# Optimization experiments

Measured on AMD Instinct MI355X. Metric: run time of the kernel, lower is better.

Reference implementation:

```python
import jax, jax.numpy as jnp
import numpy as np

N = 100000      # num_nodes
E = 1600000     # num_edges
D_IN = 256      # input_dim
H = 64          # hidden_dim
OUT = 32        # output_dim
EMB = 128       # node2vec embedding_dim
HEADS = 2       # GAT heads (concat=False -> mean over heads)
NEG_SLOPE = 0.2 # GATConv leaky_relu default


def setup_inputs() -> dict:
    key = jax.random.key(0)
    ks = jax.random.split(key, 24)
    s = lambda k, shape, fan: (jax.random.normal(k, shape, jnp.float32) * (1.0 / np.sqrt(fan)))
    return {
        "x": jax.random.normal(ks[0], (N, D_IN), jnp.float32),
        "edge_index": jax.random.randint(ks[1], (2, E), 0, N, jnp.int64),
        # frozen node2vec embedding table (used under no_grad in the original)
        "n2v_emb": jax.random.normal(ks[2], (N, EMB), jnp.float32),
        "n2v_proj_w": s(ks[3], (EMB, H), EMB), "n2v_proj_b": jnp.zeros((H,), jnp.float32),
        "input_proj_w": s(ks[4], (D_IN + H, H), D_IN + H), "input_proj_b": jnp.zeros((H,), jnp.float32),
        "gate_w": s(ks[5], (D_IN + H, H), D_IN + H), "gate_b": jnp.zeros((H,), jnp.float32),
        # SAGEConv layers: out = mean_agg(x_j) @ wl + bl + x @ wr
        "sage0_wl": s(ks[6], (H, H), H), "sage0_bl": jnp.zeros((H,), jnp.float32), "sage0_wr": s(ks[7], (H, H), H),
        "sage1_wl": s(ks[8], (H, H), H), "sage1_bl": jnp.zeros((H,), jnp.float32), "sage1_wr": s(ks[9], (H, H), H),
        # GATConv(H, H, heads=2, concat=False)
        "gat_w": s(ks[10], (H, HEADS * H), H),
        "gat_att_src": s(ks[11], (HEADS, H), H), "gat_att_dst": s(ks[12], (HEADS, H), H),
        "gat_b": jnp.zeros((H,), jnp.float32),
        "fin_wl": s(ks[13], (H, OUT), H), "fin_bl": jnp.zeros((OUT,), jnp.float32), "fin_wr": s(ks[14], (H, OUT), H),
    }


def _sage(h, src, dst, wl, bl, wr, n):
    # PyG SAGEConv with mean aggregation: lin_l(mean_j h_j) + lin_r(h_i)
    msum = jax.ops.segment_sum(h[src], dst, num_segments=n)
    deg = jax.ops.segment_sum(jnp.ones((src.shape[0],), h.dtype), dst, num_segments=n)
    agg = msum / jnp.maximum(deg, 1.0)[:, None]
    return agg @ wl + bl + h @ wr


def _gat(h, src, dst, w, att_src, att_dst, b, n):
    # GATConv with self-loops (PyG default), heads averaged (concat=False)
    loops = jnp.arange(n, dtype=src.dtype)
    src = jnp.concatenate([src, loops]); dst = jnp.concatenate([dst, loops])
    xh = (h @ w).reshape(n, HEADS, H)                     # [n, heads, H]
    a_src = jnp.einsum('nhd,hd->nh', xh, att_src)         # [n, heads]
    a_dst = jnp.einsum('nhd,hd->nh', xh, att_dst)
    e = jax.nn.leaky_relu(a_src[src] + a_dst[dst], NEG_SLOPE)  # [E', heads]
    emax = jax.ops.segment_max(e, dst, num_segments=n)
    ex = jnp.exp(e - emax[dst])
    esum = jax.ops.segment_sum(ex, dst, num_segments=n)
    alpha = ex / (esum[dst] + 1e-16)                      # edge softmax per dst, per head
    out = jax.ops.segment_sum(alpha[:, :, None] * xh[src], dst, num_segments=n)
    return out.mean(axis=1) + b                           # [n, H]


def reference(x, edge_index, n2v_emb, n2v_proj_w, n2v_proj_b, input_proj_w, input_proj_b,
              gate_w, gate_b, sage0_wl, sage0_bl, sage0_wr, sage1_wl, sage1_bl, sage1_wr,
              gat_w, gat_att_src, gat_att_dst, gat_b, fin_wl, fin_bl, fin_wr):
    n = x.shape[0]
    src, dst = edge_index[0], edge_index[1]
    # node2vec embeddings are frozen (torch.no_grad in original)
    n2v = jax.lax.stop_gradient(n2v_emb)
    n2v_p = n2v @ n2v_proj_w + n2v_proj_b                 # [n, H]
    combined = jnp.concatenate([x, n2v_p], axis=-1)       # [n, D_IN+H]
    gate = jax.nn.sigmoid(combined @ gate_w + gate_b)
    x_proj = combined @ input_proj_w + input_proj_b
    raw_proj = jnp.concatenate([x, jnp.zeros((n, H), x.dtype)], axis=-1) @ input_proj_w + input_proj_b
    h = gate * x_proj + (1.0 - gate) * raw_proj           # node_indices=None -> all nodes
    h = jax.nn.relu(_sage(h, src, dst, sage0_wl, sage0_bl, sage0_wr, n))
    h = jax.nn.relu(_sage(h, src, dst, sage1_wl, sage1_bl, sage1_wr, n))
    h = jax.nn.relu(_gat(h, src, dst, gat_w, gat_att_src, gat_att_dst, gat_b, n))
    return _sage(h, src, dst, fin_wl, fin_bl, fin_wr, n)  # [n, OUT]
```

## Files before the change

### kernel.cpp

```cpp
#include <hip/hip_runtime.h>
#include <math.h>

#define NN 100000
#define NE 1600000
#define DIN 256
#define HD 64
#define OUTD 32
#define EMBD 128
#define SLOPE 0.2f
#define AST 68
#define NT ((NN + 63) / 64)
#define SCHUNK 1024
#define SNBLK ((NN + SCHUNK - 1) / SCHUNK)

__device__ __forceinline__ float lrelu(float x) { return x > 0.f ? x : SLOPE * x; }
__device__ __forceinline__ ushort f2b(float f) {
    unsigned u = __float_as_uint(f);
    return (ushort)((u + 0x7FFFu + ((u >> 16) & 1u)) >> 16);
}
__device__ __forceinline__ float b2f(ushort v) { return __uint_as_float(((unsigned)v) << 16); }

__global__ void k_count(const int* __restrict__ dst, int* __restrict__ cnt) {
    int i = blockIdx.x * blockDim.x + threadIdx.x;
    if (i < NE) atomicAdd(&cnt[dst[i]], 1);
}

__global__ __launch_bounds__(256) void k_scan1(const int* __restrict__ cnt,
                                               int* __restrict__ rowptr,
                                               int* __restrict__ blksum) {
    __shared__ int ts[256];
    int base = blockIdx.x * SCHUNK + threadIdx.x * 4;
    int v0 = 0, v1 = 0, v2 = 0, v3 = 0;
    if (base < NN)     v0 = cnt[base];
    if (base + 1 < NN) v1 = cnt[base + 1];
    if (base + 2 < NN) v2 = cnt[base + 2];
    if (base + 3 < NN) v3 = cnt[base + 3];
    int s = v0 + v1 + v2 + v3;
    ts[threadIdx.x] = s;
    __syncthreads();
    for (int off = 1; off < 256; off <<= 1) {
        int w = (threadIdx.x >= off) ? ts[threadIdx.x - off] : 0;
        __syncthreads();
        ts[threadIdx.x] += w;
        __syncthreads();
    }
    int excl = ts[threadIdx.x] - s;
    if (base < NN)     rowptr[base]     = excl;
    if (base + 1 < NN) rowptr[base + 1] = excl + v0;
    if (base + 2 < NN) rowptr[base + 2] = excl + v0 + v1;
    if (base + 3 < NN) rowptr[base + 3] = excl + v0 + v1 + v2;
    if (threadIdx.x == 255) blksum[blockIdx.x] = ts[255];
}

__global__ __launch_bounds__(128) void k_scan2(int* __restrict__ blksum) {
    __shared__ int ts[128];
    int t = threadIdx.x;
    int v = (t < SNBLK) ? blksum[t] : 0;
    ts[t] = v;
    __syncthreads();
    for (int off = 1; off < 128; off <<= 1) {
        int w = (t >= off) ? ts[t - off] : 0;
        __syncthreads();
        ts[t] += w;
        __syncthreads();
    }
    if (t < SNBLK) blksum[t] = ts[t] - v;
}

__global__ void k_scan3(const int* __restrict__ blksum, const int* __restrict__ cnt,
                        int* __restrict__ rowptr, int* __restrict__ cursor,
                        float* __restrict__ invdeg) {
    int i = blockIdx.x * blockDim.x + threadIdx.x;
    if (i < NN) {
        int v = rowptr[i] + blksum[i >> 10];
        rowptr[i] = v;
        cursor[i] = v;
        invdeg[i] = 1.0f / fmaxf((float)cnt[i], 1.0f);
    }
    if (i == 0) rowptr[NN] = NE;
}

__global__ void k_fill(const int* __restrict__ src, const int* __restrict__ dst,
                       int* __restrict__ cursor, int* __restrict__ colsrc) {
    int i = blockIdx.x * blockDim.x + threadIdx.x;
    if (i >= NE) return;
    int pos = atomicAdd(&cursor[dst[i]], 1);
    colsrc[pos] = src[i];
}

__device__ __forceinline__ void stageA(const float* __restrict__ g, int nbase, int ldg, int koff,
                                       float (*As)[AST]) {
    for (int i = threadIdx.x; i < 1024; i += 256) {
        int m = i >> 4, k4 = (i & 15) << 2;
        int row = nbase + m;
        if (row >= NN) row = NN - 1;
        *(float4*)&As[m][k4] = *(const float4*)&g[(size_t)row * ldg + koff + k4];
    }
}
__device__ __forceinline__ void stageW(const float* __restrict__ g, float* Ws) {
    for (int i = threadIdx.x; i < 1024; i += 256) ((float4*)Ws)[i] = ((const float4*)g)[i];
}
__device__ __forceinline__ void stageWcols(const float* __restrict__ g, int ldg, int coff,
                                           float* Ws) {
    for (int i = threadIdx.x; i < 1024; i += 256) {
        int r = i >> 4, c4 = (i & 15) << 2;
        *(float4*)&Ws[r * 64 + c4] = *(const float4*)&g[r * ldg + coff + c4];
    }
}
__device__ __forceinline__ void mac16v(const float (*As)[AST], const float* __restrict__ Ws,
                                       float (*acc)[4], int tr, int tc) {
#pragma unroll 4
    for (int k4 = 0; k4 < 64; k4 += 4) {
        float4 a0 = *(const float4*)&As[tr * 4 + 0][k4];
        float4 a1 = *(const float4*)&As[tr * 4 + 1][k4];
        float4 a2 = *(const float4*)&As[tr * 4 + 2][k4];
        float4 a3 = *(const float4*)&As[tr * 4 + 3][k4];
#pragma unroll
        for (int j = 0; j < 4; j++) {
            float4 w = *(const float4*)&Ws[(k4 + j) * 64 + tc * 4];
            float e0 = (&a0.x)[j], e1 = (&a1.x)[j], e2 = (&a2.x)[j], e3 = (&a3.x)[j];
            acc[0][0] += e0 * w.x; acc[0][1] += e0 * w.y; acc[0][2] += e0 * w.z; acc[0][3] += e0 * w.w;
            acc[1][0] += e1 * w.x; acc[1][1] += e1 * w.y; acc[1][2] += e1 * w.z; acc[1][3] += e1 * w.w;
            acc[2][0] += e2 * w.x; acc[2][1] += e2 * w.y; acc[2][2] += e2 * w.z; acc[2][3] += e2 * w.w;
            acc[3][0] += e3 * w.x; acc[3][1] += e3 * w.y; acc[3][2] += e3 * w.z; acc[3][3] += e3 * w.w;
        }
    }
}

__global__ __launch_bounds__(256) void k_n2vp_t(const float* __restrict__ n2v,
                                                const float* __restrict__ w,
                                                const float* __restrict__ b,
                                                float* __restrict__ n2vp) {
    __shared__ float As[64][AST];
    __shared__ float Ws[64 * 64];
    int nbase = blockIdx.x * 64;
    int tc = threadIdx.x & 15, tr = threadIdx.x >> 4;
    float acc[4][4] = {};
    for (int c = 0; c < 2; c++) {
        if (c) __syncthreads();
        stageA(n2v, nbase, EMBD, c * 64, As);
        stageW(w + c * 64 * 64, Ws);
        __syncthreads();
        mac16v(As, Ws, acc, tr, tc);
    }
    float b0 = b[tc * 4], b1 = b[tc * 4 + 1], b2 = b[tc * 4 + 2], b3 = b[tc * 4 + 3];
#pragma unroll
    for (int i = 0; i < 4; i++) {
        int row = nbase + tr * 4 + i;
        if (row < NN) {
            float4 o = {acc[i][0] + b0, acc[i][1] + b1, acc[i][2] + b2, acc[i][3] + b3};
            *(float4*)&n2vp[(size_t)row * HD + tc * 4] = o;
        }
    }
}

__global__ __launch_bounds__(256) void k_front_t(const float* __restrict__ x,
                                                 const float* __restrict__ n2vp,
                                                 const float* __restrict__ ip_w,
                                                 const float* __restrict__ ip_b,
                                                 const float* __restrict__ gate_w,
                                                 const float* __restrict__ gate_b,
                                                 float* __restrict__ h0,
                                                 ushort* __restrict__ h0b) {
    __shared__ float As[64][AST];
    __shared__ float Ws[64 * 64];
    int nbase = blockIdx.x * 64;
    int tc = threadIdx.x & 15, tr = threadIdx.x >> 4;
    float araw[4][4] = {}, ag[4][4] = {}, adel[4][4] = {};
    for (int c = 0; c < 4; c++) {
        if (c) __syncthreads();
        stageA(x, nbase, DIN, c * 64, As);
        stageW(ip_w + c * 64 * 64, Ws);
        __syncthreads();
        mac16v(As, Ws, araw, tr, tc);
        __syncthreads();
        stageW(gate_w + c * 64 * 64, Ws);
        __syncthreads();
        mac16v(As, Ws, ag, tr, tc);
    }
    __syncthreads();
    stageA(n2vp, nbase, HD, 0, As);
    stageW(ip_w + DIN * 64, Ws);
    __syncthreads();
    mac16v(As, Ws, adel, tr, tc);
    __syncthreads();
    stageW(gate_w + DIN * 64, Ws);
    __syncthreads();
    mac16v(As, Ws, ag, tr, tc);

    float ib0 = ip_b[tc * 4], ib1 = ip_b[tc * 4 + 1], ib2 = ip_b[tc * 4 + 2], ib3 = ip_b[tc * 4 + 3];
    float gb0 = gate_b[tc * 4], gb1 = gate_b[tc * 4 + 1], gb2 = gate_b[tc * 4 + 2], gb3 = gate_b[tc * 4 + 3];
#pragma unroll
    for (int i = 0; i < 4; i++) {
        int row = nbase + tr * 4 + i;
        if (row < NN) {
            float r0 = araw[i][0] + ib0, r1 = araw[i][1] + ib1, r2 = araw[i][2] + ib2, r3 = araw[i][3] + ib3;
            float s0 = 1.f / (1.f + __expf(-(ag[i][0] + gb0)));
            float s1 = 1.f / (1.f + __expf(-(ag[i][1] + gb1)));
            float s2 = 1.f / (1.f + __expf(-(ag[i][2] + gb2)));
            float s3 = 1.f / (1.f + __expf(-(ag[i][3] + gb3)));
            float4 o = {r0 + s0 * adel[i][0], r1 + s1 * adel[i][1],
                        r2 + s2 * adel[i][2], r3 + s3 * adel[i][3]};
            *(float4*)&h0[(size_t)row * HD + tc * 4] = o;
            ushort4 ob = {f2b(o.x), f2b(o.y), f2b(o.z), f2b(o.w)};
            *(ushort4*)&h0b[(size_t)row * HD + tc * 4] = ob;
        }
    }
}

__global__ void k_gather_mean(const int* __restrict__ rowptr, const int* __restrict__ colsrc,
                              const float* __restrict__ invdeg, const ushort* __restrict__ hb,
                              float* __restrict__ agg) {
    int t = threadIdx.x & 63;
    int lane = t & 31, half = t >> 5;
    int gw = blockIdx.x * (blockDim.x >> 6) + (threadIdx.x >> 6);
    int stride = gridDim.x * (blockDim.x >> 6);
    for (int n = gw; n < NN; n += stride) {
        int bg = rowptr[n], en = rowptr[n + 1];
        float a0 = 0.f, a1 = 0.f;
        int i = bg + half;
        for (; i + 6 < en; i += 8) {
            int sa = colsrc[i], sb = colsrc[i + 2], sc = colsrc[i + 4], sd = colsrc[i + 6];
            ushort2 va = *(const ushort2*)&hb[(size_t)sa * HD + lane * 2];
            ushort2 vb = *(const ushort2*)&hb[(size_t)sb * HD + lane * 2];
            ushort2 vc = *(const ushort2*)&hb[(size_t)sc * HD + lane * 2];
            ushort2 vd = *(const ushort2*)&hb[(size_t)sd * HD + lane * 2];
            a0 += b2f(va.x) + b2f(vb.x) + b2f(vc.x) + b2f(vd.x);
            a1 += b2f(va.y) + b2f(vb.y) + b2f(vc.y) + b2f(vd.y);
        }
        for (; i < en; i += 2) {
            int s = colsrc[i];
            ushort2 v = *(const ushort2*)&hb[(size_t)s * HD + lane * 2];
            a0 += b2f(v.x);
            a1 += b2f(v.y);
        }
        a0 += __shfl_xor(a0, 32);
        a1 += __shfl_xor(a1, 32);
        if (half == 0) {
            float id = invdeg[n];
            float2 o = {a0 * id, a1 * id};
            *(float2*)&agg[(size_t)n * HD + lane * 2] = o;
        }
    }
}

__global__ __launch_bounds__(256) void k_sage_t(const float* __restrict__ agg,
                                                const float* __restrict__ h,
                                                const float* __restrict__ wl,
                                                const float* __restrict__ bl,
                                                const float* __restrict__ wr,
                                                float* __restrict__ hout,
                                                ushort* __restrict__ houtb) {
    __shared__ float As[64][AST];
    __shared__ float Ws[64 * 64];
    int nbase = blockIdx.x * 64;
    int tc = threadIdx.x & 15, tr = threadIdx.x >> 4;
    float acc[4][4] = {};
    stageA(agg, nbase, HD, 0, As);
    stageW(wl, Ws);
    __syncthreads();
    mac16v(As, Ws, acc, tr, tc);
    __syncthreads();
    stageA(h, nbase, HD, 0, As);
    stageW(wr, Ws);
    __syncthreads();
    mac16v(As, Ws, acc, tr, tc);
    float b0 = bl[tc * 4], b1 = bl[tc * 4 + 1], b2 = bl[tc * 4 + 2], b3 = bl[tc * 4 + 3];
#pragma unroll
    for (int i = 0; i < 4; i++) {
        int row = nbase + tr * 4 + i;
        if (row < NN) {
            float4 o = {fmaxf(acc[i][0] + b0, 0.f), fmaxf(acc[i][1] + b1, 0.f),
                        fmaxf(acc[i][2] + b2, 0.f), fmaxf(acc[i][3] + b3, 0.f)};
            *(float4*)&hout[(size_t)row * HD + tc * 4] = o;
            ushort4 ob = {f2b(o.x), f2b(o.y), f2b(o.z), f2b(o.w)};
            *(ushort4*)&houtb[(size_t)row * HD + tc * 4] = ob;
        }
    }
}

__global__ __launch_bounds__(256) void k_gatxh_t(const float* __restrict__ h,
                                                 const float* __restrict__ w,
                                                 const float* __restrict__ att_s,
                                                 const float* __restrict__ att_d,
                                                 ushort* __restrict__ xhb,
                                                 float* __restrict__ a_s,
                                                 float* __restrict__ a_d) {
    __shared__ float As[64][AST];
    __shared__ float Ws[64 * 64];
    int nbase = blockIdx.x * 64;
    int tc = threadIdx.x & 15, tr = threadIdx.x >> 4;
    stageA(h, nbase, HD, 0, As);
#pragma unroll
    for (int half = 0; half < 2; half++) {
        if (half) __syncthreads();
        stageWcols(w, 128, half * 64, Ws);
        __syncthreads();
        float acc[4][4] = {};
        mac16v(As, Ws, acc, tr, tc);
        float as0 = att_s[half * 64 + tc * 4], as1 = att_s[half * 64 + tc * 4 + 1];
        float as2 = att_s[half * 64 + tc * 4 + 2], as3 = att_s[half * 64 + tc * 4 + 3];
        float ad0 = att_d[half * 64 + tc * 4], ad1 = att_d[half * 64 + tc * 4 + 1];
        float ad2 = att_d[half * 64 + tc * 4 + 2], ad3 = att_d[half * 64 + tc * 4 + 3];
#pragma unroll
        for (int i = 0; i < 4; i++) {
            int row = nbase + tr * 4 + i;
            float ps = acc[i][0] * as0 + acc[i][1] * as1 + acc[i][2] * as2 + acc[i][3] * as3;
            float pd = acc[i][0] * ad0 + acc[i][1] * ad1 + acc[i][2] * ad2 + acc[i][3] * ad3;
#pragma unroll
            for (int off = 8; off; off >>= 1) {
                ps += __shfl_xor(ps, off);
                pd += __shfl_xor(pd, off);
            }
            if (row < NN) {
                ushort4 ob = {f2b(acc[i][0]), f2b(acc[i][1]), f2b(acc[i][2]), f2b(acc[i][3])};
                *(ushort4*)&xhb[(size_t)row * 128 + half * 64 + tc * 4] = ob;
                if (tc == 0) {
                    a_s[row * 2 + half] = ps;
                    a_d[row * 2 + half] = pd;
                }
            }
        }
    }
}

__global__ void k_gat_fused(const int* __restrict__ rowptr, const int* __restrict__ colsrc,
                            const float* __restrict__ a_s, const float* __restrict__ a_d,
                            const ushort* __restrict__ xhb, const float* __restrict__ gb,
                            float* __restrict__ hout) {
    int t = threadIdx.x & 63;
    int lane = t & 31, half = t >> 5;
    int bl4 = (lane & 15) * 4;
    float4 bias4 = *(const float4*)&gb[bl4];
    int gw = blockIdx.x * (blockDim.x >> 6) + (threadIdx.x >> 6);
    int stride = gridDim.x * (blockDim.x >> 6);
    for (int n = gw; n < NN; n += stride) {
        int bg = rowptr[n], en = rowptr[n + 1];
        float ad0 = a_d[n * 2], ad1 = a_d[n * 2 + 1];
        float a0 = 0.f, a1 = 0.f, a2 = 0.f, a3 = 0.f;
        float ss0 = 0.f, ss1 = 0.f;
        int i = bg + half;
        for (; i + 2 < en; i += 4) {
            int sa = colsrc[i], sb = colsrc[i + 2];
            float2 ava = *(const float2*)&a_s[sa * 2];
            float2 avb = *(const float2*)&a_s[sb * 2];
            ushort4 xva = *(const ushort4*)&xhb[(size_t)sa * 128 + lane * 4];
            ushort4 xvb = *(const ushort4*)&xhb[(size_t)sb * 128 + lane * 4];
            float wa0 = __expf(lrelu(ava.x + ad0));
            float wa1 = __expf(lrelu(ava.y + ad1));
            float wb0 = __expf(lrelu(avb.x + ad0));
            float wb1 = __expf(lrelu(avb.y + ad1));
            ss0 += wa0 + wb0;
            ss1 += wa1 + wb1;
            float wsa = (lane < 16) ? wa0 : wa1;
            float wsb = (lane < 16) ? wb0 : wb1;
            a0 += wsa * b2f(xva.x) + wsb * b2f(xvb.x);
            a1 += wsa * b2f(xva.y) + wsb * b2f(xvb.y);
            a2 += wsa * b2f(xva.z) + wsb * b2f(xvb.z);
            a3 += wsa * b2f(xva.w) + wsb * b2f(xvb.w);
        }
        for (; i < en; i += 2) {
            int s = colsrc[i];
            float2 av = *(const float2*)&a_s[s * 2];
            float w0 = __expf(lrelu(av.x + ad0));
            float w1 = __expf(lrelu(av.y + ad1));
            ss0 += w0;
            ss1 += w1;
            float wsel = (lane < 16) ? w0 : w1;
            ushort4 xv = *(const ushort4*)&xhb[(size_t)s * 128 + lane * 4];
            a0 += wsel * b2f(xv.x);
            a1 += wsel * b2f(xv.y);
            a2 += wsel * b2f(xv.z);
            a3 += wsel * b2f(xv.w);
        }
        if (half == 0) {
            float2 av = *(const float2*)&a_s[n * 2];
            float w0 = __expf(lrelu(av.x + ad0));
            float w1 = __expf(lrelu(av.y + ad1));
            ss0 += w0;
            ss1 += w1;
            float wsel = (lane < 16) ? w0 : w1;
            ushort4 xv = *(const ushort4*)&xhb[(size_t)n * 128 + lane * 4];
            a0 += wsel * b2f(xv.x);
            a1 += wsel * b2f(xv.y);
            a2 += wsel * b2f(xv.z);
            a3 += wsel * b2f(xv.w);
        }
        ss0 += __shfl_xor(ss0, 32);
        ss1 += __shfl_xor(ss1, 32);
        a0 += __shfl_xor(a0, 32);
        a1 += __shfl_xor(a1, 32);
        a2 += __shfl_xor(a2, 32);
        a3 += __shfl_xor(a3, 32);
        float r = (lane < 16) ? (0.5f / (ss0 + 1e-16f)) : (0.5f / (ss1 + 1e-16f));
        float v0 = a0 * r, v1 = a1 * r, v2 = a2 * r, v3 = a3 * r;
        float p0 = __shfl_xor(v0, 16);
        float p1 = __shfl_xor(v1, 16);
        float p2 = __shfl_xor(v2, 16);
        float p3 = __shfl_xor(v3, 16);
        if (half == 0 && lane < 16) {
            float4 o = {fmaxf(v0 + p0 + bias4.x, 0.f), fmaxf(v1 + p1 + bias4.y, 0.f),
                        fmaxf(v2 + p2 + bias4.z, 0.f), fmaxf(v3 + p3 + bias4.w, 0.f)};
            *(float4*)&hout[(size_t)n * HD + lane * 4] = o;
        }
    }
}

__global__ void k_pfin(const float* __restrict__ h, const float* __restrict__ wl,
                       ushort* __restrict__ Pb) {
    __shared__ float sw[HD * OUTD];
    for (int i = threadIdx.x; i < HD * OUTD; i += blockDim.x) sw[i] = wl[i];
    __syncthreads();
    int t = threadIdx.x & 63;
    int c = t & 31, half = t >> 5;
    int gw = blockIdx.x * (blockDim.x >> 6) + (threadIdx.x >> 6);
    int stride = gridDim.x * (blockDim.x >> 6);
    for (int n = gw; n < NN; n += stride) {
        float hv = h[(size_t)n * HD + t];
        float acc = 0.f;
#pragma unroll 8
        for (int i = 0; i < 32; i++) {
            float bb = __shfl(hv, half * 32 + i);
            acc += bb * sw[half * 1024 + i * 32 + c];
        }
        acc += __shfl_xor(acc, 32);
        if (half == 0) Pb[(size_t)n * OUTD + c] = f2b(acc);
    }
}

__global__ void k_final_fused(const int* __restrict__ rowptr, const int* __restrict__ colsrc,
                              const float* __restrict__ invdeg, const ushort* __restrict__ Pb,
                              const float* __restrict__ h, const float* __restrict__ bl,
                              const float* __restrict__ wr, float* __restrict__ out) {
    __shared__ float sw[HD * OUTD];
    for (int i = threadIdx.x; i < HD * OUTD; i += blockDim.x) sw[i] = wr[i];
    __syncthreads();
    int t = threadIdx.x & 63;
    int j = t & 31, half = t >> 5;
    int quarter = t >> 4, lane16 = t & 15;
    float bias = bl[j];
    int gw = blockIdx.x * (blockDim.x >> 6) + (threadIdx.x >> 6);
    int stride = gridDim.x * (blockDim.x >> 6);
    for (int n = gw; n < NN; n += stride) {
        int bg = rowptr[n], en = rowptr[n + 1];
        float a0 = 0.f, a1 = 0.f;
        int i = bg + quarter;
        for (; i + 4 < en; i += 8) {
            int sa = colsrc[i], sb = colsrc[i + 4];
            ushort2 va = *(const ushort2*)&Pb[(size_t)sa * OUTD + lane16 * 2];
            ushort2 vb = *(const ushort2*)&Pb[(size_t)sb * OUTD + lane16 * 2];
            a0 += b2f(va.x) + b2f(vb.x);
            a1 += b2f(va.y) + b2f(vb.y);
        }
        for (; i < en; i += 4) {
            int s = colsrc[i];
            ushort2 v = *(const ushort2*)&Pb[(size_t)s * OUTD + lane16 * 2];
            a0 += b2f(v.x);
            a1 += b2f(v.y);
        }
        a0 += __shfl_xor(a0, 32);
        a1 += __shfl_xor(a1, 32);
        a0 += __shfl_xor(a0, 16);
        a1 += __shfl_xor(a1, 16);
        float hv = h[(size_t)n * HD + t];
        float o = 0.f;
#pragma unroll 8
        for (int i2 = 0; i2 < 32; i2++) {
            float bb = __shfl(hv, half * 32 + i2);
            o += bb * sw[half * 1024 + i2 * 32 + j];
        }
        o += __shfl_xor(o, 32);
        float ga = __shfl(a0, j >> 1);
        float gb_ = __shfl(a1, j >> 1);
        float gv = (j & 1) ? gb_ : ga;
        if (half == 0) out[(size_t)n * OUTD + j] = gv * invdeg[n] + bias + o;
    }
}

extern "C" void kernel_launch(void* const* d_in, const int* in_sizes, int n_in,
                              void* d_out, int out_size, void* d_ws, size_t ws_size,
                              hipStream_t stream) {
    const float* x      = (const float*)d_in[0];
    const int*   eidx   = (const int*)d_in[1];
    const float* n2v    = (const float*)d_in[2];
    const float* n2v_w  = (const float*)d_in[3];
    const float* n2v_b  = (const float*)d_in[4];
    const float* ip_w   = (const float*)d_in[5];
    const float* ip_b   = (const float*)d_in[6];
    const float* gate_w = (const float*)d_in[7];
    const float* gate_b = (const float*)d_in[8];
    const float* s0_wl  = (const float*)d_in[9];
    const float* s0_bl  = (const float*)d_in[10];
    const float* s0_wr  = (const float*)d_in[11];
    const float* s1_wl  = (const float*)d_in[12];
    const float* s1_bl  = (const float*)d_in[13];
    const float* s1_wr  = (const float*)d_in[14];
    const float* gat_w  = (const float*)d_in[15];
    const float* att_s  = (const float*)d_in[16];
    const float* att_d  = (const float*)d_in[17];
    const float* gat_b  = (const float*)d_in[18];
    const float* f_wl   = (const float*)d_in[19];
    const float* f_bl   = (const float*)d_in[20];
    const float* f_wr   = (const float*)d_in[21];

    const int* src = eidx;
    const int* dst = eidx + NE;

    float*  ws     = (float*)d_ws;
    float*  invdeg = ws;
    float*  S1     = invdeg + NN;
    float*  S2     = S1 + (size_t)NN * HD;
    float*  SA     = S2 + (size_t)NN * HD;
    float*  a_s    = SA + (size_t)NN * HD;
    float*  a_d    = a_s + (size_t)NN * 2;
    ushort* Pb     = (ushort*)(a_d + (size_t)NN * 2);
    ushort* hb     = Pb + (size_t)NN * OUTD;
    ushort* xhb    = hb + (size_t)NN * HD;
    int*    cnt    = (int*)(xhb + (size_t)NN * 128);
    int*    rowptr = cnt + NN;
    int*    cursor = rowptr + NN + 1;
    int*    blksum = cursor + NN;
    int*    colsrc = blksum + 128;

    float* n2vp = SA;
    float* agg  = SA;
    float* out  = (float*)d_out;

    const int BT = 256;
    dim3 b128(128), b256(BT);
    int eblk = (NE + BT - 1) / BT;
    int nblk = (NN + BT - 1) / BT;

    hipMemsetAsync(cnt, 0, (size_t)NN * 4, stream);
    k_count<<<eblk, b256, 0, stream>>>(dst, cnt);
    k_scan1<<<SNBLK, b256, 0, stream>>>(cnt, rowptr, blksum);
    k_scan2<<<1, b128, 0, stream>>>(blksum);
    k_scan3<<<nblk, b256, 0, stream>>>(blksum, cnt, rowptr, cursor, invdeg);
    k_fill<<<eblk, b256, 0, stream>>>(src, dst, cursor, colsrc);

    k_n2vp_t<<<NT, b256, 0, stream>>>(n2v, n2v_w, n2v_b, n2vp);
    k_front_t<<<NT, b256, 0, stream>>>(x, n2vp, ip_w, ip_b, gate_w, gate_b, S2, hb);

    k_gather_mean<<<2048, b256, 0, stream>>>(rowptr, colsrc, invdeg, hb, agg);
    k_sage_t<<<NT, b256, 0, stream>>>(agg, S2, s0_wl, s0_bl, s0_wr, S1, hb);

    k_gather_mean<<<2048, b256, 0, stream>>>(rowptr, colsrc, invdeg, hb, agg);
    k_sage_t<<<NT, b256, 0, stream>>>(agg, S1, s1_wl, s1_bl, s1_wr, S2, hb);

    k_gatxh_t<<<NT, b256, 0, stream>>>(S2, gat_w, att_s, att_d, xhb, a_s, a_d);
    k_gat_fused<<<2048, b256, 0, stream>>>(rowptr, colsrc, a_s, a_d, xhb, gat_b, S1);

    k_pfin<<<2048, b256, 0, stream>>>(S1, f_wl, Pb);
    k_final_fused<<<2048, b256, 0, stream>>>(rowptr, colsrc, invdeg, Pb, S1, f_bl, f_wr, out);
}
```

Measured before the change: 758.0 us.

## Use split-bf16 MFMA for the front input-projection and gate GEMMs

Rewrites the front projection kernel to use 16x16x32 bf16 MFMA instructions in place of scalar FP32 multiply-accumulate. Each operand is split into a high and a low bf16 part, and three MFMAs per product (hi*hi, hi*lo, lo*hi) keep accuracy close to FP32. The goal is to take this roughly 100000x320x128 GEMM off the vector ALUs. In exchange, every block converts the weights to bf16 again, and the epilogue writes scalar values in a column-strided pattern rather than float4 rows, which may cost some store efficiency.

After: 709.3 us. 6.4% less time.

```diff
diff --git a/kernel.cpp b/kernel.cpp
--- a/kernel.cpp
+++ b/kernel.cpp
@@ -12,6 +12,10 @@
 #define NT ((NN + 63) / 64)
 #define SCHUNK 1024
 #define SNBLK ((NN + SCHUNK - 1) / SCHUNK)
+
+typedef __attribute__((ext_vector_type(8))) short bf16x8;
+typedef __attribute__((ext_vector_type(8))) unsigned short u16x8;
+typedef __attribute__((ext_vector_type(4))) float f32x4;
 
 __device__ __forceinline__ float lrelu(float x) { return x > 0.f ? x : SLOPE * x; }
 __device__ __forceinline__ ushort f2b(float f) {
@@ -162,48 +166,146 @@
                                                  const float* __restrict__ gate_b,
                                                  float* __restrict__ h0,
                                                  ushort* __restrict__ h0b) {
-    __shared__ float As[64][AST];
-    __shared__ float Ws[64 * 64];
+    __shared__ ushort Ah[64][40], Al[64][40];
+    __shared__ ushort Bih[64][40], Bil[64][40];
+    __shared__ ushort Bgh[64][40], Bgl[64][40];
     int nbase = blockIdx.x * 64;
-    int tc = threadIdx.x & 15, tr = threadIdx.x >> 4;
-    float araw[4][4] = {}, ag[4][4] = {}, adel[4][4] = {};
-    for (int c = 0; c < 4; c++) {
+    int tid = threadIdx.x;
+    int w = tid >> 6, l = tid & 63;
+    int lr = l & 15, lg = l >> 4, lk = lg * 8;
+    f32x4 zero = {0.f, 0.f, 0.f, 0.f};
+    f32x4 araw[4], ag[4], adel[4];
+#pragma unroll
+    for (int t = 0; t < 4; t++) { araw[t] = zero; ag[t] = zero; adel[t] = zero; }
+
+    int arow = tid >> 2, ak0 = (tid & 3) << 3;
+    int garow = nbase + arow;
+    if (garow >= NN) garow = NN - 1;
+
+    for (int c = 0; c < 8; c++) {
         if (c) __syncthreads();
-        stageA(x, nbase, DIN, c * 64, As);
-        stageW(ip_w + c * 64 * 64, Ws);
-        __syncthreads();
-        mac16v(As, Ws, araw, tr, tc);
-        __syncthreads();
-        stageW(gate_w + c * 64 * 64, Ws);
-        __syncthreads();
-        mac16v(As, Ws, ag, tr, tc);
-    }
-    __syncthreads();
-    stageA(n2vp, nbase, HD, 0, As);
-    stageW(ip_w + DIN * 64, Ws);
-    __syncthreads();
-    mac16v(As, Ws, adel, tr, tc);
-    __syncthreads();
-    stageW(gate_w + DIN * 64, Ws);
-    __syncthreads();
-    mac16v(As, Ws, ag, tr, tc);
-
-    float ib0 = ip_b[tc * 4], ib1 = ip_b[tc * 4 + 1], ib2 = ip_b[tc * 4 + 2], ib3 = ip_b[tc * 4 + 3];
-    float gb0 = gate_b[tc * 4], gb1 = gate_b[tc * 4 + 1], gb2 = gate_b[tc * 4 + 2], gb3 = gate_b[tc * 4 + 3];
-#pragma unroll
-    for (int i = 0; i < 4; i++) {
-        int row = nbase + tr * 4 + i;
-        if (row < NN) {
-            float r0 = araw[i][0] + ib0, r1 = araw[i][1] + ib1, r2 = araw[i][2] + ib2, r3 = araw[i][3] + ib3;
-            float s0 = 1.f / (1.f + __expf(-(ag[i][0] + gb0)));
-            float s1 = 1.f / (1.f + __expf(-(ag[i][1] + gb1)));
-            float s2 = 1.f / (1.f + __expf(-(ag[i][2] + gb2)));
-            float s3 = 1.f / (1.f + __expf(-(ag[i][3] + gb3)));
-            float4 o = {r0 + s0 * adel[i][0], r1 + s1 * adel[i][1],
-                        r2 + s2 * adel[i][2], r3 + s3 * adel[i][3]};
-            *(float4*)&h0[(size_t)row * HD + tc * 4] = o;
-            ushort4 ob = {f2b(o.x), f2b(o.y), f2b(o.z), f2b(o.w)};
-            *(ushort4*)&h0b[(size_t)row * HD + tc * 4] = ob;
+        {
+            const float* src = &x[(size_t)garow * DIN + c * 32 + ak0];
+            u16x8 th, tl;
+#pragma unroll
+            for (int u = 0; u < 8; u++) {
+                float v = src[u];
+                ushort h = f2b(v);
+                th[u] = h;
+                tl[u] = f2b(v - b2f(h));
+            }
+            *(u16x8*)&Ah[arow][ak0] = th;
+            *(u16x8*)&Al[arow][ak0] = tl;
+        }
+        {
+            const float* pi = &ip_w[(size_t)(c * 32 + w * 8) * 64 + l];
+            const float* pg = &gate_w[(size_t)(c * 32 + w * 8) * 64 + l];
+            u16x8 ih, il, gh, gl2;
+#pragma unroll
+            for (int u = 0; u < 8; u++) {
+                float v = pi[u * 64];
+                ushort h = f2b(v);
+                ih[u] = h; il[u] = f2b(v - b2f(h));
+                float g = pg[u * 64];
+                ushort hg = f2b(g);
+                gh[u] = hg; gl2[u] = f2b(g - b2f(hg));
+            }
+            *(u16x8*)&Bih[l][w * 8] = ih;
+            *(u16x8*)&Bil[l][w * 8] = il;
+            *(u16x8*)&Bgh[l][w * 8] = gh;
+            *(u16x8*)&Bgl[l][w * 8] = gl2;
+        }
+        __syncthreads();
+        bf16x8 ah = *(const bf16x8*)&Ah[w * 16 + lr][lk];
+        bf16x8 al = *(const bf16x8*)&Al[w * 16 + lr][lk];
+#pragma unroll
+        for (int t = 0; t < 4; t++) {
+            int col = t * 16 + lr;
+            bf16x8 bih = *(const bf16x8*)&Bih[col][lk];
+            bf16x8 bil = *(const bf16x8*)&Bil[col][lk];
+            bf16x8 bgh = *(const bf16x8*)&Bgh[col][lk];
+            bf16x8 bgl = *(const bf16x8*)&Bgl[col][lk];
+            f32x4 r = araw[t];
+            r = __builtin_amdgcn_mfma_f32_16x16x32_bf16(ah, bih, r, 0, 0, 0);
+            r = __builtin_amdgcn_mfma_f32_16x16x32_bf16(ah, bil, r, 0, 0, 0);
+            r = __builtin_amdgcn_mfma_f32_16x16x32_bf16(al, bih, r, 0, 0, 0);
+            araw[t] = r;
+            f32x4 g = ag[t];
+            g = __builtin_amdgcn_mfma_f32_16x16x32_bf16(ah, bgh, g, 0, 0, 0);
+            g = __builtin_amdgcn_mfma_f32_16x16x32_bf16(ah, bgl, g, 0, 0, 0);
+            g = __builtin_amdgcn_mfma_f32_16x16x32_bf16(al, bgh, g, 0, 0, 0);
+            ag[t] = g;
+        }
+    }
+    for (int c = 0; c < 2; c++) {
+        __syncthreads();
+        {
+            const float* src = &n2vp[(size_t)garow * HD + c * 32 + ak0];
+            u16x8 th, tl;
+#pragma unroll
+            for (int u = 0; u < 8; u++) {
+                float v = src[u];
+                ushort h = f2b(v);
+                th[u] = h;
+                tl[u] = f2b(v - b2f(h));
+            }
+            *(u16x8*)&Ah[arow][ak0] = th;
+            *(u16x8*)&Al[arow][ak0] = tl;
+        }
+        {
+            const float* pi = &ip_w[(size_t)(DIN + c * 32 + w * 8) * 64 + l];
+            const float* pg = &gate_w[(size_t)(DIN + c * 32 + w * 8) * 64 + l];
+            u16x8 ih, il, gh, gl2;
+#pragma unroll
+            for (int u = 0; u < 8; u++) {
+                float v = pi[u * 64];
+                ushort h = f2b(v);
+                ih[u] = h; il[u] = f2b(v - b2f(h));
+                float g = pg[u * 64];
+                ushort hg = f2b(g);
+                gh[u] = hg; gl2[u] = f2b(g - b2f(hg));
+            }
+            *(u16x8*)&Bih[l][w * 8] = ih;
+            *(u16x8*)&Bil[l][w * 8] = il;
+            *(u16x8*)&Bgh[l][w * 8] = gh;
+            *(u16x8*)&Bgl[l][w * 8] = gl2;
+        }
+        __syncthreads();
+        bf16x8 ah = *(const bf16x8*)&Ah[w * 16 + lr][lk];
+        bf16x8 al = *(const bf16x8*)&Al[w * 16 + lr][lk];
+#pragma unroll
+        for (int t = 0; t < 4; t++) {
+            int col = t * 16 + lr;
+            bf16x8 bih = *(const bf16x8*)&Bih[col][lk];
+            bf16x8 bil = *(const bf16x8*)&Bil[col][lk];
+            bf16x8 bgh = *(const bf16x8*)&Bgh[col][lk];
+            bf16x8 bgl = *(const bf16x8*)&Bgl[col][lk];
+            f32x4 r = adel[t];
+            r = __builtin_amdgcn_mfma_f32_16x16x32_bf16(ah, bih, r, 0, 0, 0);
+            r = __builtin_amdgcn_mfma_f32_16x16x32_bf16(ah, bil, r, 0, 0, 0);
+            r = __builtin_amdgcn_mfma_f32_16x16x32_bf16(al, bih, r, 0, 0, 0);
+            adel[t] = r;
+            f32x4 g = ag[t];
+            g = __builtin_amdgcn_mfma_f32_16x16x32_bf16(ah, bgh, g, 0, 0, 0);
+            g = __builtin_amdgcn_mfma_f32_16x16x32_bf16(ah, bgl, g, 0, 0, 0);
+            g = __builtin_amdgcn_mfma_f32_16x16x32_bf16(al, bgh, g, 0, 0, 0);
+            ag[t] = g;
+        }
+    }
+#pragma unroll
+    for (int t = 0; t < 4; t++) {
+        int col = t * 16 + lr;
+        float ib = ip_b[col], gb2 = gate_b[col];
+#pragma unroll
+        for (int r = 0; r < 4; r++) {
+            int row = nbase + w * 16 + lg * 4 + r;
+            if (row < NN) {
+                float raw = araw[t][r] + ib;
+                float sg = 1.f / (1.f + __expf(-(ag[t][r] + gb2)));
+                float o = raw + sg * adel[t][r];
+                h0[(size_t)row * HD + col] = o;
+                h0b[(size_t)row * HD + col] = f2b(o);
+            }
         }
     }
 }
```
